# Kernel optimization log

Hardware: AMD Instinct MI355X
Metric: run time of the kernel (lower is better)

Reference implementation:

```python
import jax, jax.numpy as jnp
import numpy as np

TMP = 1.0  # temperature from init

def setup_inputs() -> dict:
    key = jax.random.key(0)
    k1, k2, k3 = jax.random.split(key, 3)
    B, D, C = 8192, 1024, 4096
    x = jax.random.normal(k1, (B, D), dtype=jnp.float32)
    mod = jax.random.normal(k2, (B, D), dtype=jnp.float32)
    W = jax.random.normal(k3, (C, D), dtype=jnp.float32) * 0.02  # cls.weight
    return {"x": x, "mod": mod, "W": W}

def reference(x, mod, W):
    # att = softmax(mod / tmp, axis=1) + 1, shape (B, D)
    att = jax.nn.softmax(mod / TMP, axis=1) + 1.0
    # result[b, c] = sum_d W[c, d] * att[b, d] * x[b, d]
    # == (att * x) @ W.T  -- collapses the repeat + per-sample matvec loop
    return jnp.einsum('bd,cd->bc', att * x, W)
```

## Files before the change

### kernel.cpp

```cpp
#include <hip/hip_runtime.h>
#include <hip/hip_bf16.h>
#include <cstdint>
#include <cstddef>

typedef __bf16 bf16_t;
typedef __bf16 bf16x8 __attribute__((ext_vector_type(8)));
typedef __bf16 bf16x4 __attribute__((ext_vector_type(4)));
typedef float  f32x4  __attribute__((ext_vector_type(4)));

#define BM 128
#define BN 128
#define BK 64

__global__ void att_scale_kernel(const float* __restrict__ x,
                                 const float* __restrict__ mod,
                                 bf16_t* __restrict__ a, int D) {
  const int b = blockIdx.x;
  const int t = threadIdx.x;
  const size_t row = (size_t)b * D;

  float4 mv = ((const float4*)(mod + row))[t];
  float mx = fmaxf(fmaxf(mv.x, mv.y), fmaxf(mv.z, mv.w));
#pragma unroll
  for (int o = 32; o > 0; o >>= 1) mx = fmaxf(mx, __shfl_xor(mx, o));

  __shared__ float redmax[4];
  __shared__ float redsum[4];
  const int wave = t >> 6, lane = t & 63;
  if (lane == 0) redmax[wave] = mx;
  __syncthreads();
  mx = fmaxf(fmaxf(redmax[0], redmax[1]), fmaxf(redmax[2], redmax[3]));

  float4 e;
  e.x = __expf(mv.x - mx); e.y = __expf(mv.y - mx);
  e.z = __expf(mv.z - mx); e.w = __expf(mv.w - mx);
  float s = (e.x + e.y) + (e.z + e.w);
#pragma unroll
  for (int o = 32; o > 0; o >>= 1) s += __shfl_xor(s, o);
  if (lane == 0) redsum[wave] = s;
  __syncthreads();
  s = (redsum[0] + redsum[1]) + (redsum[2] + redsum[3]);

  const float inv = 1.0f / s;
  float4 xv = ((const float4*)(x + row))[t];
  bf16x4 o4;
  o4[0] = (bf16_t)((e.x * inv + 1.0f) * xv.x);
  o4[1] = (bf16_t)((e.y * inv + 1.0f) * xv.y);
  o4[2] = (bf16_t)((e.z * inv + 1.0f) * xv.z);
  o4[3] = (bf16_t)((e.w * inv + 1.0f) * xv.w);
  *((bf16x4*)(a + row) + t) = o4;
}

__global__ void cast_w_kernel(const float* __restrict__ W,
                              bf16_t* __restrict__ Wb) {
  const size_t i = ((size_t)blockIdx.x * blockDim.x + threadIdx.x) * 8;
  float4 u = *(const float4*)(W + i);
  float4 v = *(const float4*)(W + i + 4);
  bf16x8 o;
  o[0] = (bf16_t)u.x; o[1] = (bf16_t)u.y; o[2] = (bf16_t)u.z; o[3] = (bf16_t)u.w;
  o[4] = (bf16_t)v.x; o[5] = (bf16_t)v.y; o[6] = (bf16_t)v.z; o[7] = (bf16_t)v.w;
  *(bf16x8*)(Wb + i) = o;
}

__global__ __launch_bounds__(256) void gemm_bt_kernel(
    const bf16_t* __restrict__ A, const bf16_t* __restrict__ B,
    float* __restrict__ C, int M, int N, int K) {
  __shared__ __align__(16) bf16_t As[BM * BK];
  __shared__ __align__(16) bf16_t Bs[BN * BK];

  const int tid  = threadIdx.x;
  const int wave = tid >> 6;
  const int lane = tid & 63;
  const int quad = lane >> 4;
  const int l16  = lane & 15;

  const int m0 = blockIdx.y * BM;
  const int n0 = blockIdx.x * BN;
  const int wm = wave & 1;
  const int wn = wave >> 1;

  f32x4 acc[4][4];
#pragma unroll
  for (int i = 0; i < 4; i++)
#pragma unroll
    for (int j = 0; j < 4; j++) acc[i][j] = (f32x4){0.f, 0.f, 0.f, 0.f};

  const int rowA    = tid >> 3;
  const int col8swz = (tid & 7) ^ (rowA & 7);
  const bf16_t* aptr = A + (size_t)(m0 + rowA) * K + col8swz * 8;
  const bf16_t* bptr = B + (size_t)(n0 + rowA) * K + col8swz * 8;

  for (int k0 = 0; k0 < K; k0 += BK) {
#pragma unroll
    for (int i = 0; i < 4; i++) {
      __builtin_amdgcn_global_load_lds(
          (const __attribute__((address_space(1))) void*)(aptr + (size_t)(i * 32) * K + k0),
          (__attribute__((address_space(3))) void*)(As + (i * 256 + wave * 64) * 8),
          16, 0, 0);
    }
#pragma unroll
    for (int i = 0; i < 4; i++) {
      __builtin_amdgcn_global_load_lds(
          (const __attribute__((address_space(1))) void*)(bptr + (size_t)(i * 32) * K + k0),
          (__attribute__((address_space(3))) void*)(Bs + (i * 256 + wave * 64) * 8),
          16, 0, 0);
    }
    __syncthreads();

#pragma unroll
    for (int kt = 0; kt < 2; kt++) {
      bf16x8 af[4], bf[4];
#pragma unroll
      for (int i = 0; i < 4; i++) {
        const int r = wm * 64 + i * 16 + l16;
        const int c8 = ((kt << 2) | quad) ^ (l16 & 7);
        af[i] = *(const bf16x8*)&As[r * BK + c8 * 8];
      }
#pragma unroll
      for (int j = 0; j < 4; j++) {
        const int r = wn * 64 + j * 16 + l16;
        const int c8 = ((kt << 2) | quad) ^ (l16 & 7);
        bf[j] = *(const bf16x8*)&Bs[r * BK + c8 * 8];
      }
#pragma unroll
      for (int i = 0; i < 4; i++)
#pragma unroll
        for (int j = 0; j < 4; j++)
          acc[i][j] = __builtin_amdgcn_mfma_f32_16x16x32_bf16(af[i], bf[j], acc[i][j], 0, 0, 0);
    }
    __syncthreads();
  }

#pragma unroll
  for (int i = 0; i < 4; i++) {
    const int mg = m0 + wm * 64 + i * 16 + quad * 4;
#pragma unroll
    for (int j = 0; j < 4; j++) {
      const int ng = n0 + wn * 64 + j * 16 + l16;
#pragma unroll
      for (int r = 0; r < 4; r++) {
        C[(size_t)(mg + r) * N + ng] = acc[i][j][r];
      }
    }
  }
}

extern "C" void kernel_launch(void* const* d_in, const int* in_sizes, int n_in,
                              void* d_out, int out_size, void* d_ws, size_t ws_size,
                              hipStream_t stream) {
  const float* x   = (const float*)d_in[0];
  const float* mod = (const float*)d_in[1];
  const float* W   = (const float*)d_in[2];
  float* out = (float*)d_out;

  const int D = 1024;
  const int Bn = in_sizes[0] / D;
  const int Cn = in_sizes[2] / D;

  bf16_t* a  = (bf16_t*)d_ws;
  bf16_t* Wb = (bf16_t*)((char*)d_ws + (size_t)Bn * D * sizeof(bf16_t));

  att_scale_kernel<<<Bn, 256, 0, stream>>>(x, mod, a, D);
  cast_w_kernel<<<((size_t)Cn * D) / (256 * 8), 256, 0, stream>>>(W, Wb);
  gemm_bt_kernel<<<dim3(Cn / BN, Bn / BM), 256, 0, stream>>>(a, Wb, out, Bn, Cn, D);
}
```

Measured before the change: 265.3 us.

## Rewrite GEMM as 256x256 tile with double-buffered LDS pipeline and XCD remap

Replaces the 128x128 single-buffered GEMM with a 512-thread 256x256 tile kernel. It double-buffers LDS, issues next-tile global-to-LDS loads interleaved across four compute phases with fine-grained waitcnt and barriers, and uses s_setprio around the MFMA bursts. Block indices are remapped across 8 XCD groups so neighbouring tiles share L2. The goal is to hide global load latency and raise arithmetic intensity. In exchange, register and LDS use grow (128KB LDS), K is hardcoded to 1024, and the grid tail may be uneven.

```diff
diff --git a/kernel.cpp b/kernel.cpp
--- a/kernel.cpp
+++ b/kernel.cpp
@@ -8,9 +8,8 @@
 typedef __bf16 bf16x4 __attribute__((ext_vector_type(4)));
 typedef float  f32x4  __attribute__((ext_vector_type(4)));
 
-#define BM 128
-#define BN 128
-#define BK 64
+#define KDIM 1024
+#define NT   16
 
 __global__ void att_scale_kernel(const float* __restrict__ x,
                                  const float* __restrict__ mod,
@@ -62,85 +61,124 @@
   *(bf16x8*)(Wb + i) = o;
 }
 
-__global__ __launch_bounds__(256) void gemm_bt_kernel(
+__global__ __launch_bounds__(512, 2) void gemm256_kernel(
     const bf16_t* __restrict__ A, const bf16_t* __restrict__ B,
-    float* __restrict__ C, int M, int N, int K) {
-  __shared__ __align__(16) bf16_t As[BM * BK];
-  __shared__ __align__(16) bf16_t Bs[BN * BK];
+    float* __restrict__ C, int M, int N) {
+  __shared__ __align__(16) bf16_t lds[2 * 32768];
 
   const int tid  = threadIdx.x;
   const int wave = tid >> 6;
   const int lane = tid & 63;
   const int quad = lane >> 4;
   const int l16  = lane & 15;
-
-  const int m0 = blockIdx.y * BM;
-  const int n0 = blockIdx.x * BN;
-  const int wm = wave & 1;
-  const int wn = wave >> 1;
-
-  f32x4 acc[4][4];
-#pragma unroll
-  for (int i = 0; i < 4; i++)
-#pragma unroll
-    for (int j = 0; j < 4; j++) acc[i][j] = (f32x4){0.f, 0.f, 0.f, 0.f};
-
-  const int rowA    = tid >> 3;
-  const int col8swz = (tid & 7) ^ (rowA & 7);
-  const bf16_t* aptr = A + (size_t)(m0 + rowA) * K + col8swz * 8;
-  const bf16_t* bptr = B + (size_t)(n0 + rowA) * K + col8swz * 8;
-
-  for (int k0 = 0; k0 < K; k0 += BK) {
-#pragma unroll
-    for (int i = 0; i < 4; i++) {
-      __builtin_amdgcn_global_load_lds(
-          (const __attribute__((address_space(1))) void*)(aptr + (size_t)(i * 32) * K + k0),
-          (__attribute__((address_space(3))) void*)(As + (i * 256 + wave * 64) * 8),
-          16, 0, 0);
+  const int wm   = wave >> 2;
+  const int wn   = wave & 3;
+
+  const int nwg = gridDim.x;
+  int flat = blockIdx.x;
+  flat = (flat & 7) * (nwg >> 3) + (flat >> 3);
+  const int ntiles = N >> 8;
+  const int m0 = (flat / ntiles) << 8;
+  const int n0 = (flat % ntiles) << 8;
+
+  const int trow = tid >> 3;
+  const int colg = (tid & 7) ^ (trow & 7);
+  const bf16_t* aSrc = A + (size_t)(m0 + trow) * KDIM + colg * 8;
+  const bf16_t* bSrc = B + (size_t)(n0 + trow) * KDIM + colg * 8;
+  const int ldsW = wave * 512;
+
+#define GLDS(src_, dst_) __builtin_amdgcn_global_load_lds( \
+      (const __attribute__((address_space(1))) void*)(src_), \
+      (__attribute__((address_space(3))) void*)(dst_), 16, 0, 0)
+
+#define ISSUE_A(h, u_) do { \
+      const bf16_t* s_ = aSrc + (size_t)((h) * 128) * KDIM + (u_) * 64; \
+      bf16_t* d_ = lds + ((u_) & 1) * 32768 + (h) * 8192 + ldsW; \
+      GLDS(s_, d_); \
+      GLDS(s_ + (size_t)64 * KDIM, d_ + 4096); \
+    } while (0)
+
+#define ISSUE_B(h, u_) do { \
+      const bf16_t* s_ = bSrc + (size_t)((h) * 128) * KDIM + (u_) * 64; \
+      bf16_t* d_ = lds + ((u_) & 1) * 32768 + 16384 + (h) * 8192 + ldsW; \
+      GLDS(s_, d_); \
+      GLDS(s_ + (size_t)64 * KDIM, d_ + 4096); \
+    } while (0)
+
+  ISSUE_A(0, 0); ISSUE_A(1, 0);
+  ISSUE_B(0, 0); ISSUE_B(1, 0);
+  ISSUE_B(0, 1); ISSUE_B(1, 1);
+
+  f32x4 acc[8][4];
+#pragma unroll
+  for (int i = 0; i < 8; ++i)
+#pragma unroll
+    for (int j = 0; j < 4; ++j) acc[i][j] = (f32x4){0.f, 0.f, 0.f, 0.f};
+
+  const int aBase = (wm * 128 + l16) * 64;
+  const int bBase = (wn * 64 + l16) * 64;
+  const int c0 = ((quad)     ^ (l16 & 7)) * 8;
+  const int c1 = ((4 + quad) ^ (l16 & 7)) * 8;
+
+  asm volatile("s_waitcnt vmcnt(4)" ::: "memory");
+  __builtin_amdgcn_s_barrier();
+
+  bf16x8 bfr[4][2];
+
+#define PHASE(q_, ISSUE_STMT, WAIT_STMT) do { \
+      bf16x8 af[2][2]; \
+      _Pragma("unroll") \
+      for (int i = 0; i < 2; ++i) { \
+        af[i][0] = *(const bf16x8*)(At + aBase + ((q_) * 32 + i * 16) * 64 + c0); \
+        af[i][1] = *(const bf16x8*)(At + aBase + ((q_) * 32 + i * 16) * 64 + c1); \
+      } \
+      ISSUE_STMT; \
+      asm volatile("" ::: "memory"); \
+      __builtin_amdgcn_s_barrier(); \
+      asm volatile("s_waitcnt lgkmcnt(0)" ::: "memory"); \
+      __builtin_amdgcn_s_setprio(1); \
+      _Pragma("unroll") \
+      for (int i = 0; i < 2; ++i) \
+        _Pragma("unroll") \
+        for (int j = 0; j < 4; ++j) { \
+          acc[(q_) * 2 + i][j] = __builtin_amdgcn_mfma_f32_16x16x32_bf16( \
+              af[i][0], bfr[j][0], acc[(q_) * 2 + i][j], 0, 0, 0); \
+          acc[(q_) * 2 + i][j] = __builtin_amdgcn_mfma_f32_16x16x32_bf16( \
+              af[i][1], bfr[j][1], acc[(q_) * 2 + i][j], 0, 0, 0); \
+        } \
+      __builtin_amdgcn_s_setprio(0); \
+      WAIT_STMT; \
+      asm volatile("" ::: "memory"); \
+      __builtin_amdgcn_s_barrier(); \
+    } while (0)
+
+#pragma unroll 1
+  for (int u = 0; u < NT; ++u) {
+    const bf16_t* At = lds + (u & 1) * 32768;
+    const bf16_t* Bt = At + 16384;
+
+#pragma unroll
+    for (int j = 0; j < 4; ++j) {
+      bfr[j][0] = *(const bf16x8*)(Bt + bBase + j * 16 * 64 + c0);
+      bfr[j][1] = *(const bf16x8*)(Bt + bBase + j * 16 * 64 + c1);
     }
-#pragma unroll
-    for (int i = 0; i < 4; i++) {
-      __builtin_amdgcn_global_load_lds(
-          (const __attribute__((address_space(1))) void*)(bptr + (size_t)(i * 32) * K + k0),
-          (__attribute__((address_space(3))) void*)(Bs + (i * 256 + wave * 64) * 8),
-          16, 0, 0);
-    }
-    __syncthreads();
-
-#pragma unroll
-    for (int kt = 0; kt < 2; kt++) {
-      bf16x8 af[4], bf[4];
-#pragma unroll
-      for (int i = 0; i < 4; i++) {
-        const int r = wm * 64 + i * 16 + l16;
-        const int c8 = ((kt << 2) | quad) ^ (l16 & 7);
-        af[i] = *(const bf16x8*)&As[r * BK + c8 * 8];
-      }
-#pragma unroll
-      for (int j = 0; j < 4; j++) {
-        const int r = wn * 64 + j * 16 + l16;
-        const int c8 = ((kt << 2) | quad) ^ (l16 & 7);
-        bf[j] = *(const bf16x8*)&Bs[r * BK + c8 * 8];
-      }
-#pragma unroll
-      for (int i = 0; i < 4; i++)
-#pragma unroll
-        for (int j = 0; j < 4; j++)
-          acc[i][j] = __builtin_amdgcn_mfma_f32_16x16x32_bf16(af[i], bf[j], acc[i][j], 0, 0, 0);
-    }
-    __syncthreads();
+    PHASE(0, if (u + 1 < NT) ISSUE_A(0, u + 1), (void)0);
+    PHASE(1, if (u + 1 < NT) ISSUE_A(1, u + 1), (void)0);
+    PHASE(2, if (u + 2 < NT) ISSUE_B(0, u + 2), (void)0);
+    PHASE(3, if (u + 2 < NT) ISSUE_B(1, u + 2),
+          if (u < NT - 2) { asm volatile("s_waitcnt vmcnt(4)" ::: "memory"); }
+          else            { asm volatile("s_waitcnt vmcnt(0)" ::: "memory"); });
   }
 
 #pragma unroll
-  for (int i = 0; i < 4; i++) {
-    const int mg = m0 + wm * 64 + i * 16 + quad * 4;
-#pragma unroll
-    for (int j = 0; j < 4; j++) {
+  for (int ri = 0; ri < 8; ++ri) {
+    const int mg = m0 + wm * 128 + ri * 16 + quad * 4;
+#pragma unroll
+    for (int j = 0; j < 4; ++j) {
       const int ng = n0 + wn * 64 + j * 16 + l16;
 #pragma unroll
-      for (int r = 0; r < 4; r++) {
-        C[(size_t)(mg + r) * N + ng] = acc[i][j][r];
-      }
+      for (int r = 0; r < 4; ++r)
+        C[(size_t)(mg + r) * N + ng] = acc[ri][j][r];
     }
   }
 }
@@ -162,5 +200,7 @@
 
   att_scale_kernel<<<Bn, 256, 0, stream>>>(x, mod, a, D);
   cast_w_kernel<<<((size_t)Cn * D) / (256 * 8), 256, 0, stream>>>(W, Wb);
-  gemm_bt_kernel<<<dim3(Cn / BN, Bn / BM), 256, 0, stream>>>(a, Wb, out, Bn, Cn, D);
-}
+
+  const int nwg = (Bn / 256) * (Cn / 256);
+  gemm256_kernel<<<nwg, 512, 0, stream>>>(a, Wb, out, Bn, Cn);
+}
```

New measurement: 257.0 us. 1.03x faster.
